# Performance work log

Hardware: AMD Instinct MI355X
Metric: run time of the kernel (lower is better)

## Reference

```python
import jax, jax.numpy as jnp
import numpy as np

MAX_ITER = 3
DAMPING = 1e-3


def _sobel(img):
    # img: (H, W, C). Replicate pad + torch-style cross-correlation with Sobel kernels.
    p = jnp.pad(img, ((1, 1), (1, 1), (0, 0)), mode='edge')
    dx = (-p[:-2, :-2] + p[:-2, 2:]
          - 2.0 * p[1:-1, :-2] + 2.0 * p[1:-1, 2:]
          - p[2:, :-2] + p[2:, 2:])
    dy = (-p[:-2, :-2] - 2.0 * p[:-2, 1:-1] - p[:-2, 2:]
          + p[2:, :-2] + 2.0 * p[2:, 1:-1] + p[2:, 2:])
    return dx, dy


def _compute_vertex(depth, K):
    H, W = depth.shape
    fx, fy, cx, cy = K[0, 0], K[1, 1], K[0, 2], K[1, 2]
    j, i = jnp.meshgrid(jnp.arange(H, dtype=depth.dtype),
                        jnp.arange(W, dtype=depth.dtype), indexing='ij')
    dirs = jnp.stack([(i - cx) / fx, (j - cy) / fy, jnp.ones_like(i)], axis=-1)
    return dirs * depth[..., None]  # (H, W, 3)


def _compute_normal(vmap):
    dx, dy = _sobel(vmap)  # unnormalized gradients (normalize_gradient=False)
    n = jnp.cross(dx.reshape(-1, 3), dy.reshape(-1, 3)).reshape(vmap.shape)
    n = n / (jnp.linalg.norm(n, axis=-1, keepdims=True) + 1e-8)
    depth = vmap[..., -1]
    invalid = (depth <= depth.min()) | (depth >= depth.max())
    return jnp.where(invalid[..., None], 0.0, n)


def _warp_bilinear(feat, u, v):
    # grid_sample(mode='bilinear', padding_mode='border', align_corners=True):
    # with u_norm = u/((W-1)/2)-1 the sample location is exactly pixel (u, v).
    H, W, C = feat.shape
    uc = jnp.clip(u, 0.0, W - 1.0)
    vc = jnp.clip(v, 0.0, H - 1.0)
    x0 = jnp.floor(uc)
    y0 = jnp.floor(vc)
    x0i = x0.astype(jnp.int32)
    y0i = y0.astype(jnp.int32)
    x1i = jnp.minimum(x0i + 1, W - 1)
    y1i = jnp.minimum(y0i + 1, H - 1)
    wx = (uc - x0)[..., None]
    wy = (vc - y0)[..., None]
    f00 = feat[y0i, x0i]
    f01 = feat[y0i, x1i]
    f10 = feat[y1i, x0i]
    f11 = feat[y1i, x1i]
    top = f00 * (1.0 - wx) + f01 * wx
    bot = f10 * (1.0 - wx) + f11 * wx
    return top * (1.0 - wy) + bot * wy


def _exp_so3(w):
    eps = 1e-10
    o = jnp.zeros((), dtype=w.dtype)
    w_hat = jnp.stack([o, -w[2], w[1], w[2], o, -w[0], -w[1], w[0], o]).reshape(3, 3)
    w_hat2 = w_hat @ w_hat
    theta = jnp.linalg.norm(w)
    safe = jnp.where(theta <= eps, 1.0, theta)
    eye3 = jnp.eye(3, dtype=w.dtype)
    e_w = eye3 + w_hat * (jnp.sin(theta) / safe) + w_hat2 * ((1.0 - jnp.cos(theta)) / (safe * safe))
    return jnp.where(theta <= eps, eye3, e_w)


def _residuals_jacobian(vertex0, vertex1, normal0, normal1, mask0, pose10, K):
    H, W, _ = vertex0.shape
    R = pose10[:3, :3]
    t = pose10[:3, 3]
    v0to1 = (vertex0.reshape(-1, 3) @ R.T + t).reshape(H, W, 3)
    n0to1 = (normal0.reshape(-1, 3) @ R.T).reshape(H, W, 3)
    fx, fy, cx, cy = K[0, 0], K[1, 1], K[0, 2], K[1, 2]
    x_, y_, z_ = v0to1[..., 0], v0to1[..., 1], v0to1[..., 2]
    u_ = x_ / z_ * fx + cx
    v_ = y_ / z_ * fy + cy
    inviews = (u_ > 0) & (u_ < W - 1) & (v_ > 0) & (v_ < H - 1)
    r_vertex1 = _warp_bilinear(vertex1, u_, v_)
    r_normal1 = _warp_bilinear(normal1, u_, v_)
    mask1 = r_vertex1[..., -1] > 0.0
    diff = v0to1 - r_vertex1
    occ = (~inviews) | (jnp.linalg.norm(diff, axis=-1) > 0.1)
    res = (r_normal1 * diff).sum(axis=-1)  # point-to-plane residual (H, W)
    J_trs = r_normal1.reshape(-1, 3)
    # -n^T [v]_x  ==  cross(v, n)
    J_rot = jnp.cross(v0to1.reshape(-1, 3), J_trs)
    J = jnp.concatenate([J_rot, J_trs], axis=-1).reshape(H, W, 6)
    bad = occ | (~mask0) | (~mask1)
    J = jnp.where(bad[..., None], 0.0, J)
    res = jnp.where(bad, 0.0, res)
    J = -J.reshape(-1, 6)  # direction == 'forward'
    return res.reshape(-1), J


def _gn_update(JtWJ, JtR, pose, damping):
    diag = jnp.eye(6, dtype=JtWJ.dtype)
    Hess = JtWJ + jnp.trace(JtWJ) * damping * diag  # lev_mar_H
    xi = (jnp.linalg.inv(Hess) @ JtR).reshape(-1)   # least_square_solve
    d_R = _exp_so3(xi[:3])
    d_t = xi[3:]
    R = pose[:3, :3]
    t = pose[:3, 3]
    pose = pose.at[:3, :3].set(d_R @ R)
    pose = pose.at[:3, 3].set(d_R @ t + d_t)
    return pose


def _icp(pose10, depth0, depth1, K):
    vertex0 = _compute_vertex(depth0, K)
    normal0 = _compute_normal(vertex0)
    mask0 = depth0 > 0.0
    vertex1 = _compute_vertex(depth1, K)
    normal1 = _compute_normal(vertex1)
    for _ in range(MAX_ITER):
        res, J = _residuals_jacobian(vertex0, vertex1, normal0, normal1, mask0, pose10, K)
        JtWJ = jnp.einsum('ni,nj->ij', J, J)       # 6x6
        JtR = jnp.einsum('ni,n->i', J, res)[:, None]  # 6x1
        pose10 = _gn_update(JtWJ, JtR, pose10, DAMPING)
    return pose10


def setup_inputs() -> dict:
    key = jax.random.key(0)
    k0, k1 = jax.random.split(key)
    H, W = 1080, 1920
    depth0 = jax.random.uniform(k0, (H, W), jnp.float32, 0.5, 5.0)
    depth1 = depth0 + 0.01 * jax.random.normal(k1, (H, W), dtype=jnp.float32)
    K = jnp.array([[1000.0, 0.0, 960.0],
                   [0.0, 1000.0, 540.0],
                   [0.0, 0.0, 1.0]], dtype=jnp.float32)
    d_R = _exp_so3(jnp.array([0.01, -0.02, 0.01], dtype=jnp.float32))
    pose10 = jnp.eye(4, dtype=jnp.float32)
    pose10 = pose10.at[:3, :3].set(d_R)
    pose10 = pose10.at[:3, 3].set(jnp.array([0.02, -0.01, 0.03], dtype=jnp.float32))
    return {'pose10': pose10, 'depth0': depth0, 'depth1': depth1, 'K': K}


def reference(pose10, depth0, depth1, K):
    return _icp(pose10, depth0, depth1, K)
```

## Files before the change

kernel.cpp:

```cpp
#include <hip/hip_runtime.h>
#include <math.h>

#define H_IMG 1080
#define W_IMG 1920
#define NPIX (H_IMG * W_IMG)
#define QUADS (NPIX / 4)
#define NB_NM 8100
#define RB_REAL 2025
#define NACC 27

#define OFF_POSE     0
#define OFF_MINMAX   64
#define OFF_COUNT    128
#define OFF_SUMS     192
#define OFF_PARTIALS 1024
#define OFF_ND       524288

typedef _Float16 h4 __attribute__((ext_vector_type(4)));
typedef _Float16 h8 __attribute__((ext_vector_type(8)));

#define ACC_LIST(X) \
    X(0,s00) X(1,s01) X(2,s02) X(3,s03) X(4,s04) X(5,s05) \
    X(6,s11) X(7,s12) X(8,s13) X(9,s14) X(10,s15) \
    X(11,s22) X(12,s23) X(13,s24) X(14,s25) \
    X(15,s33) X(16,s34) X(17,s35) \
    X(18,s44) X(19,s45) X(20,s55) \
    X(21,b0) X(22,b1) X(23,b2) X(24,b3) X(25,b4) X(26,b5)

__device__ __forceinline__ int swz_bid(int orig, int nwg) {
    int q = nwg >> 3, r = nwg & 7;
    int xcd = orig & 7, lid = orig >> 3;
    return (xcd < r) ? xcd * (q + 1) + lid : r * (q + 1) + (xcd - r) * q + lid;
}

__global__ void k_init(const float* __restrict__ pose_in, float* __restrict__ ws_pose,
                       unsigned int* __restrict__ minmax, unsigned int* __restrict__ counter) {
    int t = threadIdx.x;
    if (t < 16) ws_pose[t] = pose_in[t];
    if (t == 16) { minmax[0] = 0x7F800000u; minmax[1] = 0u; }
    if (t == 17) *counter = 0u;
}

__global__ void k_minmax(const float4* __restrict__ dq, unsigned int* __restrict__ minmax) {
    int tid = blockIdx.x * blockDim.x + threadIdx.x;
    int stride = gridDim.x * blockDim.x;
    float mn = INFINITY, mx = -INFINITY;
    for (int i = tid; i < QUADS; i += stride) {
        float4 v = dq[i];
        mn = fminf(mn, fminf(fminf(v.x, v.y), fminf(v.z, v.w)));
        mx = fmaxf(mx, fmaxf(fmaxf(v.x, v.y), fmaxf(v.z, v.w)));
    }
    for (int off = 32; off > 0; off >>= 1) {
        mn = fminf(mn, __shfl_down(mn, off));
        mx = fmaxf(mx, __shfl_down(mx, off));
    }
    __shared__ float smn[4], smx[4];
    int lane = threadIdx.x & 63, wid = threadIdx.x >> 6;
    if (lane == 0) { smn[wid] = mn; smx[wid] = mx; }
    __syncthreads();
    if (threadIdx.x == 0) {
        for (int w = 1; w < 4; w++) { mn = fminf(mn, smn[w]); mx = fmaxf(mx, smx[w]); }
        atomicMin(&minmax[0], __float_as_uint(mn));
        atomicMax(&minmax[1], __float_as_uint(mx));
    }
}

__global__ __launch_bounds__(256)
void k_nm(const float* __restrict__ depth1, const float* __restrict__ Kmat,
          const unsigned int* __restrict__ minmax, h4* __restrict__ nd) {
    float fx = Kmat[0], cx = Kmat[2], fy = Kmat[4], cy = Kmat[5];
    float ifx = 1.f / fx, ify = 1.f / fy;
    float dmin = __uint_as_float(minmax[0]), dmax = __uint_as_float(minmax[1]);
    int idx = blockIdx.x * 256 + threadIdx.x;
    int j = idx / W_IMG;
    int i = idx - j * W_IMG;
    int r0 = j > 0 ? j - 1 : 0;
    int r2 = j < H_IMG - 1 ? j + 1 : H_IMG - 1;
    int il = i > 0 ? i - 1 : 0;
    int ir = i < W_IMG - 1 ? i + 1 : W_IMG - 1;
    const float* rp0 = depth1 + (size_t)r0 * W_IMG;
    const float* rp1 = depth1 + (size_t)j * W_IMG;
    const float* rp2 = depth1 + (size_t)r2 * W_IMG;
    float d00 = rp0[il], d01 = rp0[i], d02 = rp0[ir];
    float d10 = rp1[il], d11 = rp1[i], d12 = rp1[ir];
    float d20 = rp2[il], d21 = rp2[i], d22 = rp2[ir];
    float c0 = ((float)il - cx) * ifx, c1 = ((float)i - cx) * ifx, c2 = ((float)ir - cx) * ifx;
    float w0 = ((float)r0 - cy) * ify, w1 = ((float)j - cy) * ify, w2 = ((float)r2 - cy) * ify;
    float dxx = -c0 * d00 + c2 * d02 - 2.f * (c0 * d10) + 2.f * (c2 * d12) - c0 * d20 + c2 * d22;
    float dxy = -w0 * d00 + w0 * d02 - 2.f * (w1 * d10) + 2.f * (w1 * d12) - w2 * d20 + w2 * d22;
    float dxz = -d00 + d02 - 2.f * d10 + 2.f * d12 - d20 + d22;
    float dyx = -c0 * d00 - 2.f * (c1 * d01) - c2 * d02 + c0 * d20 + 2.f * (c1 * d21) + c2 * d22;
    float dyy = -w0 * d00 - 2.f * (w0 * d01) - w0 * d02 + w2 * d20 + 2.f * (w2 * d21) + w2 * d22;
    float dyz = -d00 - 2.f * d01 - d02 + d20 + 2.f * d21 + d22;
    float nx = dxy * dyz - dxz * dyy;
    float ny = dxz * dyx - dxx * dyz;
    float nz = dxx * dyy - dxy * dyx;
    float inv = 1.f / (sqrtf(nx * nx + ny * ny + nz * nz) + 1e-8f);
    bool invalid = (d11 <= dmin) || (d11 >= dmax);
    float s = invalid ? 0.f : inv;
    h4 e;
    e[0] = (_Float16)d11;
    e[1] = (_Float16)(nx * s);
    e[2] = (_Float16)(ny * s);
    e[3] = (_Float16)(nz * s);
    nd[idx] = e;
}

__global__ __launch_bounds__(256, 4)
void k_resid(const float* __restrict__ depth0, const float* __restrict__ Kmat,
             const h4* __restrict__ nd, const float* __restrict__ pose,
             float* __restrict__ partials) {
    float fx = Kmat[0], cx = Kmat[2], fy = Kmat[4], cy = Kmat[5];
    float ifx = 1.f / fx, ify = 1.f / fy;
    float R00 = pose[0], R01 = pose[1], R02 = pose[2],  t0 = pose[3];
    float R10 = pose[4], R11 = pose[5], R12 = pose[6],  t1 = pose[7];
    float R20 = pose[8], R21 = pose[9], R22 = pose[10], t2 = pose[11];

#define ACC_DECL(i, n) float n = 0.f;
    ACC_LIST(ACC_DECL)
#undef ACC_DECL

    int tid = threadIdx.x;
    int wg = swz_bid(blockIdx.x, gridDim.x);
    int base = wg * 1024;

    float d0s[4];
#pragma unroll
    for (int p = 0; p < 4; p++) d0s[p] = depth0[base + p * 256 + tid];

    float px[4], py[4], pz[4], wx[4], wy[4];
    int x0[4], y0[4];
    bool inview[4];
#pragma unroll
    for (int p = 0; p < 4; p++) {
        int idx = base + p * 256 + tid;
        int j = idx / W_IMG;
        int i = idx - j * W_IMG;
        float d0 = d0s[p];
        float cX = ((float)i - cx) * ifx;
        float cY = ((float)j - cy) * ify;
        float ax = R00 * cX + R01 * cY + R02;
        float ay = R10 * cX + R11 * cY + R12;
        float az = R20 * cX + R21 * cY + R22;
        float X = ax * d0 + t0;
        float Y = ay * d0 + t1;
        float Z = az * d0 + t2;
        float u, v; bool iv;
        if (Z > 1e-6f) {
            float rz = __builtin_amdgcn_rcpf(Z);
            u = X * rz * fx + cx;
            v = Y * rz * fy + cy;
            iv = (u > 0.f) && (u < (float)(W_IMG - 1)) && (v > 0.f) && (v < (float)(H_IMG - 1));
        } else { u = 0.f; v = 0.f; iv = false; }
        float x0f = floorf(u), y0f = floorf(v);
        x0[p] = (int)x0f; y0[p] = (int)y0f;
        wx[p] = u - x0f; wy[p] = v - y0f;
        px[p] = X; py[p] = Y; pz[p] = Z; inview[p] = iv;
    }
    h8 T[4], B[4];
    const h8 zz = {(_Float16)0.f, (_Float16)0.f, (_Float16)0.f, (_Float16)0.f,
                   (_Float16)0.f, (_Float16)0.f, (_Float16)0.f, (_Float16)0.f};
#pragma unroll
    for (int p = 0; p < 4; p++) {
        if (inview[p]) {
            size_t b00 = (size_t)(y0[p] * W_IMG + x0[p]);
            T[p] = *reinterpret_cast<const h8*>(nd + b00);
            B[p] = *reinterpret_cast<const h8*>(nd + b00 + W_IMG);
        } else { T[p] = zz; B[p] = zz; }
    }
#pragma unroll
    for (int p = 0; p < 4; p++) {
        _Float16 hy = (_Float16)wy[p], h1y = (_Float16)(1.f - wy[p]);
        h8 vwy = {hy, hy, hy, hy, hy, hy, hy, hy};
        h8 v1y = {h1y, h1y, h1y, h1y, h1y, h1y, h1y, h1y};
        h8 V = T[p] * v1y + B[p] * vwy;
        float w1x = 1.f - wx[p];
        float dv0 = (float)V[0], dv1 = (float)V[4];
        float rvz = dv0 * w1x + dv1 * wx[p];
        float rnx = (float)V[1] * w1x + (float)V[5] * wx[p];
        float rny = (float)V[2] * w1x + (float)V[6] * wx[p];
        float rnz = (float)V[3] * w1x + (float)V[7] * wx[p];
        float cX0 = ((float)x0[p] - cx) * ifx;
        float cY0 = ((float)y0[p] - cy) * ify;
        float rvx = cX0 * dv0 * w1x + (cX0 + ifx) * dv1 * wx[p];
        float dY0 = cY0 * (1.f - wy[p]), dY1 = (cY0 + ify) * wy[p];
        float d00 = (float)T[p][0], d01 = (float)T[p][4];
        float d10 = (float)B[p][0], d11 = (float)B[p][4];
        float rvy = (dY0 * d00 + dY1 * d10) * w1x + (dY0 * d01 + dY1 * d11) * wx[p];
        bool mask1 = rvz > 0.f;
        float ddx = px[p] - rvx, ddy = py[p] - rvy, ddz = pz[p] - rvz;
        float n2 = ddx * ddx + ddy * ddy + ddz * ddz;
        bool occ = (!inview[p]) || (n2 > 0.01f);
        bool bad = occ || !(d0s[p] > 0.f) || (!mask1);
        if (!bad) {
            float r = rnx * ddx + rny * ddy + rnz * ddz;
            float j0 = -(py[p] * rnz - pz[p] * rny);
            float j1 = -(pz[p] * rnx - px[p] * rnz);
            float j2 = -(px[p] * rny - py[p] * rnx);
            float j3 = -rnx, j4 = -rny, j5 = -rnz;
            s00 += j0 * j0; s01 += j0 * j1; s02 += j0 * j2; s03 += j0 * j3; s04 += j0 * j4; s05 += j0 * j5;
            s11 += j1 * j1; s12 += j1 * j2; s13 += j1 * j3; s14 += j1 * j4; s15 += j1 * j5;
            s22 += j2 * j2; s23 += j2 * j3; s24 += j2 * j4; s25 += j2 * j5;
            s33 += j3 * j3; s34 += j3 * j4; s35 += j3 * j5;
            s44 += j4 * j4; s45 += j4 * j5;
            s55 += j5 * j5;
            b0 += j0 * r; b1 += j1 * r; b2 += j2 * r;
            b3 += j3 * r; b4 += j4 * r; b5 += j5 * r;
        }
    }

    __shared__ float red[NACC][64];
    __shared__ float part2[NACC][8];
#define ACC_RED(i, n) { float v = n; v += __shfl_xor(v, 1); v += __shfl_xor(v, 2); \
                        if ((tid & 3) == 0) red[i][tid >> 2] = v; }
    ACC_LIST(ACC_RED)
#undef ACC_RED
    __syncthreads();
    if (tid < NACC * 8) {
        int k = tid >> 3, seg = tid & 7;
        const float4* row = reinterpret_cast<const float4*>(&red[k][seg * 8]);
        float4 a = row[0], b = row[1];
        part2[k][seg] = (a.x + a.y + a.z + a.w) + (b.x + b.y + b.z + b.w);
    }
    __syncthreads();
    if (tid < NACC) {
        float s = 0.f;
#pragma unroll
        for (int m = 0; m < 8; m++) s += part2[tid][m];
        partials[(size_t)tid * RB_REAL + blockIdx.x] = s;
    }
}

__global__ __launch_bounds__(256)
void k_reduce_solve(const float* __restrict__ partials, double* __restrict__ sums,
                    unsigned int* __restrict__ counter, float* __restrict__ pose,
                    float* __restrict__ pose_out) {
    int k = blockIdx.x;
    int tid = threadIdx.x;
    double v = 0.0;
    for (int i = tid; i < RB_REAL; i += 256) v += (double)partials[(size_t)k * RB_REAL + i];
    for (int off = 32; off > 0; off >>= 1) v += __shfl_down(v, off);
    __shared__ double sw[4];
    __shared__ int amLast;
    int lane = tid & 63, wid = tid >> 6;
    if (lane == 0) sw[wid] = v;
    __syncthreads();
    if (tid == 0) {
        sums[k] = sw[0] + sw[1] + sw[2] + sw[3];
        __threadfence();
        unsigned int old = atomicAdd(counter, 1u);
        amLast = (old == NACC - 1) ? 1 : 0;
    }
    __syncthreads();
    if (!amLast) return;
    __threadfence();

    if (tid == 0) {
        double ssum[NACC];
        for (int q = 0; q < NACC; q++) ssum[q] = sums[q];
        double sM[6][7];
        int kk = 0;
        for (int a = 0; a < 6; a++)
            for (int c = a; c < 6; c++) {
                double s = ssum[kk++];
                sM[a][c] = s; sM[c][a] = s;
            }
        double tr = sM[0][0] + sM[1][1] + sM[2][2] + sM[3][3] + sM[4][4] + sM[5][5];
        for (int a = 0; a < 6; a++) sM[a][a] += tr * 0.001;
        for (int a = 0; a < 6; a++) sM[a][6] = ssum[21 + a];
        for (int c = 0; c < 6; c++) {
            int piv = c;
            double best = fabs(sM[c][c]);
            for (int r = c + 1; r < 6; r++) {
                double vv = fabs(sM[r][c]);
                if (vv > best) { best = vv; piv = r; }
            }
            if (piv != c)
                for (int q = c; q < 7; q++) { double t = sM[c][q]; sM[c][q] = sM[piv][q]; sM[piv][q] = t; }
            double pv = sM[c][c];
            for (int r = 0; r < 6; r++) {
                if (r == c) continue;
                double f = sM[r][c] / pv;
                for (int q = c; q < 7; q++) sM[r][q] -= f * sM[c][q];
            }
        }
        double xi0 = sM[0][6] / sM[0][0], xi1 = sM[1][6] / sM[1][1], xi2 = sM[2][6] / sM[2][2];
        double xi3 = sM[3][6] / sM[3][3], xi4 = sM[4][6] / sM[4][4], xi5 = sM[5][6] / sM[5][5];
        double th = sqrt(xi0 * xi0 + xi1 * xi1 + xi2 * xi2);
        double dR[3][3] = {{1, 0, 0}, {0, 1, 0}, {0, 0, 1}};
        if (th > 1e-10) {
            double sA = sin(th) / th;
            double sB = (1.0 - cos(th)) / (th * th);
            double wh[3][3] = {{0, -xi2, xi1}, {xi2, 0, -xi0}, {-xi1, xi0, 0}};
#pragma unroll
            for (int r = 0; r < 3; r++)
#pragma unroll
                for (int cc = 0; cc < 3; cc++) {
                    double w2 = 0;
#pragma unroll
                    for (int m = 0; m < 3; m++) w2 += wh[r][m] * wh[m][cc];
                    dR[r][cc] = (r == cc ? 1.0 : 0.0) + sA * wh[r][cc] + sB * w2;
                }
        }
        double R[3][3], t[3];
#pragma unroll
        for (int r = 0; r < 3; r++) {
#pragma unroll
            for (int cc = 0; cc < 3; cc++) R[r][cc] = pose[r * 4 + cc];
            t[r] = pose[r * 4 + 3];
        }
        double xt[3] = {xi3, xi4, xi5};
#pragma unroll
        for (int r = 0; r < 3; r++) {
#pragma unroll
            for (int cc = 0; cc < 3; cc++) {
                double s = 0;
#pragma unroll
                for (int m = 0; m < 3; m++) s += dR[r][m] * R[m][cc];
                pose[r * 4 + cc] = (float)s;
            }
            pose[r * 4 + 3] = (float)(dR[r][0] * t[0] + dR[r][1] * t[1] + dR[r][2] * t[2] + xt[r]);
        }
        *counter = 0u;
        for (int q = 0; q < 16; q++) pose_out[q] = pose[q];
    }
}

extern "C" void kernel_launch(void* const* d_in, const int* in_sizes, int n_in,
                              void* d_out, int out_size, void* d_ws, size_t ws_size,
                              hipStream_t stream) {
    const float* pose_in = (const float*)d_in[0];
    const float* depth0 = (const float*)d_in[1];
    const float* depth1 = (const float*)d_in[2];
    const float* K = (const float*)d_in[3];
    float* out = (float*)d_out;
    char* ws = (char*)d_ws;
    float* ws_pose = (float*)(ws + OFF_POSE);
    unsigned int* minmax = (unsigned int*)(ws + OFF_MINMAX);
    unsigned int* counter = (unsigned int*)(ws + OFF_COUNT);
    double* sums = (double*)(ws + OFF_SUMS);
    float* partials = (float*)(ws + OFF_PARTIALS);
    h4* nd = (h4*)(ws + OFF_ND);

    k_init<<<1, 64, 0, stream>>>(pose_in, ws_pose, minmax, counter);
    k_minmax<<<1024, 256, 0, stream>>>((const float4*)depth1, minmax);
    k_nm<<<NB_NM, 256, 0, stream>>>(depth1, K, minmax, nd);
    for (int it = 0; it < 3; ++it) {
        k_resid<<<RB_REAL, 256, 0, stream>>>(depth0, K, nd, ws_pose, partials);
        k_reduce_solve<<<NACC, 256, 0, stream>>>(partials, sums, counter, ws_pose, out);
    }
}
```

Measured before the change: 129.6 us.

## Fuse depth min/max reduction into normal-map kernel and apply validity mask lazily

Removes the separate min/max pass over depth1 by computing the block min/max inside k_nm with atomics. Because the global min/max is not known while normals are written, the invalid-pixel mask is now applied in k_resid by comparing each gathered fp16 depth against dmin/dmax. This saves one full read of depth1 and a kernel launch, but adds per-sample compares and masking in all three residual passes. Comparing fp16-rounded depths against fp32 extremes may mark pixels differently than before. A Taylor-series path for small rotation angles is also added to the solve.

```diff
diff --git a/kernel.cpp b/kernel.cpp
--- a/kernel.cpp
+++ b/kernel.cpp
@@ -4,7 +4,6 @@
 #define H_IMG 1080
 #define W_IMG 1920
 #define NPIX (H_IMG * W_IMG)
-#define QUADS (NPIX / 4)
 #define NB_NM 8100
 #define RB_REAL 2025
 #define NACC 27
@@ -41,36 +40,11 @@
     if (t == 17) *counter = 0u;
 }
 
-__global__ void k_minmax(const float4* __restrict__ dq, unsigned int* __restrict__ minmax) {
-    int tid = blockIdx.x * blockDim.x + threadIdx.x;
-    int stride = gridDim.x * blockDim.x;
-    float mn = INFINITY, mx = -INFINITY;
-    for (int i = tid; i < QUADS; i += stride) {
-        float4 v = dq[i];
-        mn = fminf(mn, fminf(fminf(v.x, v.y), fminf(v.z, v.w)));
-        mx = fmaxf(mx, fmaxf(fmaxf(v.x, v.y), fmaxf(v.z, v.w)));
-    }
-    for (int off = 32; off > 0; off >>= 1) {
-        mn = fminf(mn, __shfl_down(mn, off));
-        mx = fmaxf(mx, __shfl_down(mx, off));
-    }
-    __shared__ float smn[4], smx[4];
-    int lane = threadIdx.x & 63, wid = threadIdx.x >> 6;
-    if (lane == 0) { smn[wid] = mn; smx[wid] = mx; }
-    __syncthreads();
-    if (threadIdx.x == 0) {
-        for (int w = 1; w < 4; w++) { mn = fminf(mn, smn[w]); mx = fmaxf(mx, smx[w]); }
-        atomicMin(&minmax[0], __float_as_uint(mn));
-        atomicMax(&minmax[1], __float_as_uint(mx));
-    }
-}
-
 __global__ __launch_bounds__(256)
 void k_nm(const float* __restrict__ depth1, const float* __restrict__ Kmat,
-          const unsigned int* __restrict__ minmax, h4* __restrict__ nd) {
+          h4* __restrict__ nd, unsigned int* __restrict__ minmax) {
     float fx = Kmat[0], cx = Kmat[2], fy = Kmat[4], cy = Kmat[5];
     float ifx = 1.f / fx, ify = 1.f / fy;
-    float dmin = __uint_as_float(minmax[0]), dmax = __uint_as_float(minmax[1]);
     int idx = blockIdx.x * 256 + threadIdx.x;
     int j = idx / W_IMG;
     int i = idx - j * W_IMG;
@@ -96,25 +70,40 @@
     float ny = dxz * dyx - dxx * dyz;
     float nz = dxx * dyy - dxy * dyx;
     float inv = 1.f / (sqrtf(nx * nx + ny * ny + nz * nz) + 1e-8f);
-    bool invalid = (d11 <= dmin) || (d11 >= dmax);
-    float s = invalid ? 0.f : inv;
     h4 e;
     e[0] = (_Float16)d11;
-    e[1] = (_Float16)(nx * s);
-    e[2] = (_Float16)(ny * s);
-    e[3] = (_Float16)(nz * s);
+    e[1] = (_Float16)(nx * inv);
+    e[2] = (_Float16)(ny * inv);
+    e[3] = (_Float16)(nz * inv);
     nd[idx] = e;
+
+    float mn = d11, mx = d11;
+    for (int off = 32; off > 0; off >>= 1) {
+        mn = fminf(mn, __shfl_down(mn, off));
+        mx = fmaxf(mx, __shfl_down(mx, off));
+    }
+    __shared__ float smn[4], smx[4];
+    int lane = threadIdx.x & 63, wid = threadIdx.x >> 6;
+    if (lane == 0) { smn[wid] = mn; smx[wid] = mx; }
+    __syncthreads();
+    if (threadIdx.x == 0) {
+        for (int w = 1; w < 4; w++) { mn = fminf(mn, smn[w]); mx = fmaxf(mx, smx[w]); }
+        atomicMin(&minmax[0], __float_as_uint(mn));
+        atomicMax(&minmax[1], __float_as_uint(mx));
+    }
 }
 
 __global__ __launch_bounds__(256, 4)
 void k_resid(const float* __restrict__ depth0, const float* __restrict__ Kmat,
-             const h4* __restrict__ nd, const float* __restrict__ pose,
-             float* __restrict__ partials) {
+             const h4* __restrict__ nd, const unsigned int* __restrict__ minmax,
+             const float* __restrict__ pose, float* __restrict__ partials) {
     float fx = Kmat[0], cx = Kmat[2], fy = Kmat[4], cy = Kmat[5];
     float ifx = 1.f / fx, ify = 1.f / fy;
     float R00 = pose[0], R01 = pose[1], R02 = pose[2],  t0 = pose[3];
     float R10 = pose[4], R11 = pose[5], R12 = pose[6],  t1 = pose[7];
     float R20 = pose[8], R21 = pose[9], R22 = pose[10], t2 = pose[11];
+    float dmin = __uint_as_float(minmax[0]);
+    float dmax = __uint_as_float(minmax[1]);
 
 #define ACC_DECL(i, n) float n = 0.f;
     ACC_LIST(ACC_DECL)
@@ -170,22 +159,30 @@
     }
 #pragma unroll
     for (int p = 0; p < 4; p++) {
+        float d00 = (float)T[p][0], d01 = (float)T[p][4];
+        float d10 = (float)B[p][0], d11 = (float)B[p][4];
+        const _Float16 one = (_Float16)1.f, nil = (_Float16)0.f;
+        _Float16 m00 = ((d00 <= dmin) || (d00 >= dmax)) ? nil : one;
+        _Float16 m01 = ((d01 <= dmin) || (d01 >= dmax)) ? nil : one;
+        _Float16 m10 = ((d10 <= dmin) || (d10 >= dmax)) ? nil : one;
+        _Float16 m11 = ((d11 <= dmin) || (d11 >= dmax)) ? nil : one;
+        h8 mT = {one, m00, m00, m00, one, m01, m01, m01};
+        h8 mB = {one, m10, m10, m10, one, m11, m11, m11};
         _Float16 hy = (_Float16)wy[p], h1y = (_Float16)(1.f - wy[p]);
         h8 vwy = {hy, hy, hy, hy, hy, hy, hy, hy};
         h8 v1y = {h1y, h1y, h1y, h1y, h1y, h1y, h1y, h1y};
-        h8 V = T[p] * v1y + B[p] * vwy;
+        h8 V = (T[p] * mT) * v1y + (B[p] * mB) * vwy;
         float w1x = 1.f - wx[p];
-        float dv0 = (float)V[0], dv1 = (float)V[4];
-        float rvz = dv0 * w1x + dv1 * wx[p];
+        float rvz = d00 * (1.f - wy[p]) * w1x + d01 * (1.f - wy[p]) * wx[p]
+                  + d10 * wy[p] * w1x + d11 * wy[p] * wx[p];
         float rnx = (float)V[1] * w1x + (float)V[5] * wx[p];
         float rny = (float)V[2] * w1x + (float)V[6] * wx[p];
         float rnz = (float)V[3] * w1x + (float)V[7] * wx[p];
         float cX0 = ((float)x0[p] - cx) * ifx;
         float cY0 = ((float)y0[p] - cy) * ify;
+        float dv0 = (float)V[0], dv1 = (float)V[4];
         float rvx = cX0 * dv0 * w1x + (cX0 + ifx) * dv1 * wx[p];
         float dY0 = cY0 * (1.f - wy[p]), dY1 = (cY0 + ify) * wy[p];
-        float d00 = (float)T[p][0], d01 = (float)T[p][4];
-        float d10 = (float)B[p][0], d11 = (float)B[p][4];
         float rvy = (dY0 * d00 + dY1 * d10) * w1x + (dY0 * d01 + dY1 * d11) * wx[p];
         bool mask1 = rvz > 0.f;
         float ddx = px[p] - rvx, ddy = py[p] - rvy, ddz = pz[p] - rvz;
@@ -286,11 +283,19 @@
         }
         double xi0 = sM[0][6] / sM[0][0], xi1 = sM[1][6] / sM[1][1], xi2 = sM[2][6] / sM[2][2];
         double xi3 = sM[3][6] / sM[3][3], xi4 = sM[4][6] / sM[4][4], xi5 = sM[5][6] / sM[5][5];
-        double th = sqrt(xi0 * xi0 + xi1 * xi1 + xi2 * xi2);
+        double th2 = xi0 * xi0 + xi1 * xi1 + xi2 * xi2;
+        double th = sqrt(th2);
         double dR[3][3] = {{1, 0, 0}, {0, 1, 0}, {0, 0, 1}};
         if (th > 1e-10) {
-            double sA = sin(th) / th;
-            double sB = (1.0 - cos(th)) / (th * th);
+            double sA, sB;
+            if (th < 0.5) {
+                double t4 = th2 * th2, t6 = t4 * th2;
+                sA = 1.0 - th2 / 6.0 + t4 / 120.0 - t6 / 5040.0;
+                sB = 0.5 - th2 / 24.0 + t4 / 720.0 - t6 / 40320.0;
+            } else {
+                sA = sin(th) / th;
+                sB = (1.0 - cos(th)) / th2;
+            }
             double wh[3][3] = {{0, -xi2, xi1}, {xi2, 0, -xi0}, {-xi1, xi0, 0}};
 #pragma unroll
             for (int r = 0; r < 3; r++)
@@ -343,10 +348,9 @@
     h4* nd = (h4*)(ws + OFF_ND);
 
     k_init<<<1, 64, 0, stream>>>(pose_in, ws_pose, minmax, counter);
-    k_minmax<<<1024, 256, 0, stream>>>((const float4*)depth1, minmax);
-    k_nm<<<NB_NM, 256, 0, stream>>>(depth1, K, minmax, nd);
+    k_nm<<<NB_NM, 256, 0, stream>>>(depth1, K, nd, minmax);
     for (int it = 0; it < 3; ++it) {
-        k_resid<<<RB_REAL, 256, 0, stream>>>(depth0, K, nd, ws_pose, partials);
+        k_resid<<<RB_REAL, 256, 0, stream>>>(depth0, K, nd, minmax, ws_pose, partials);
         k_reduce_solve<<<NACC, 256, 0, stream>>>(partials, sums, counter, ws_pose, out);
     }
 }
```

Result: slower. 282.7 us (+118.1%).
